# Optimization experiments

Hardware: AMD Instinct MI355X
Metric: run time of the kernel (lower is better)

The kernel has to match this reference:

```python
import jax, jax.numpy as jnp
import numpy as np

BETA, HIDDEN, C_DIM = 512, 512, 256
HP, WP, B = 64, 64, 64


def setup_inputs() -> dict:
    key = jax.random.key(0)
    ks = jax.random.split(key, 8)
    s = 0.02
    return {
        "V": jax.random.normal(ks[0], (HP, WP, C_DIM, B), dtype=jnp.float32),
        "h_t": jax.random.normal(ks[1], (B, 1, HIDDEN), dtype=jnp.float32),
        "W_h_w": jax.random.normal(ks[2], (BETA, HIDDEN), dtype=jnp.float32) * s,
        "W_h_b": jax.random.normal(ks[3], (BETA,), dtype=jnp.float32) * s,
        "W_w": jax.random.normal(ks[4], (BETA, C_DIM), dtype=jnp.float32) * s,
        "W_b": jax.random.normal(ks[5], (BETA,), dtype=jnp.float32) * s,
        "beta_w": jax.random.normal(ks[6], (1, BETA), dtype=jnp.float32) * s,
        "beta_b": jax.random.normal(ks[7], (1,), dtype=jnp.float32) * s,
    }


def reference(V, h_t, W_h_w, W_h_b, W_w, W_b, beta_w, beta_b):
    Hp, Wp, C, batch = V.shape
    # [B, HW, C]
    V_new = jnp.transpose(V, (3, 0, 1, 2)).reshape(batch, Hp * Wp, C)
    # U_T = W_h(h_t) + W(V_new): [B,1,beta] + [B,HW,beta]
    U_T = (h_t @ W_h_w.T + W_h_b) + (V_new @ W_w.T + W_b)
    # E_t: [B, HW, 1]
    E_t = jnp.tanh(U_T) @ beta_w.T + beta_b
    # softmax over the HW positions (dim=1), then transpose -> [B, 1, HW]
    A_t = jax.nn.softmax(E_t, axis=1)
    # weighted sum: [B, 1, C]
    C_T = jnp.einsum('bsk,bsc->bkc', A_t, V_new)
    return C_T
```

## Files before the change

### kernel.cpp

```cpp
#include <hip/hip_runtime.h>

typedef float f32x4 __attribute__((ext_vector_type(4)));
typedef short s16x8 __attribute__((ext_vector_type(8)));
typedef unsigned int u32;
typedef u32 u32x4 __attribute__((ext_vector_type(4)));
typedef unsigned long long u64;
typedef unsigned short ush;

#define CD    256
#define NB    64
#define NBETA 512
#define NHID  512
#define PPB   32

__device__ __forceinline__ ush f2bf(float x) {
    u32 u = __builtin_bit_cast(u32, x);
    u += 0x7fffu + ((u >> 16) & 1u);
    return (ush)(u >> 16);
}
__device__ __forceinline__ float bf2f(ush h) {
    u32 u = ((u32)h) << 16;
    return __builtin_bit_cast(float, u);
}
__device__ __forceinline__ u32 cvtpk(float lo, float hi) {
    u32 r;
    asm("v_cvt_pk_bf16_f32 %0, %1, %2" : "=v"(r) : "v"(lo), "v"(hi));
    return r;
}
__device__ __forceinline__ float fexp2(float x) {
    float r;
    asm("v_exp_f32 %0, %1" : "=v"(r) : "v"(x));
    return r;
}

__global__ __launch_bounds__(512) void prep_kernel(
    const float* __restrict__ h_t, const float* __restrict__ W_h_w,
    const float* __restrict__ W_h_b, const float* __restrict__ W_w,
    const float* __restrict__ W_b,
    ush* __restrict__ hws, ush* __restrict__ wwb)
{
    const int blk = blockIdx.x;
    const int tid = threadIdx.x;
    if (blk < NB) {
        __shared__ float hrow[NHID];
        hrow[tid] = h_t[blk * NHID + tid];
        __syncthreads();
        const float* wr = W_h_w + tid * NHID;
        float a0 = 0.f, a1 = 0.f, a2 = 0.f, a3 = 0.f;
        #pragma unroll 4
        for (int h = 0; h < NHID; h += 4) {
            f32x4 wv = *(const f32x4*)(wr + h);
            a0 = fmaf(wv.x, hrow[h], a0);
            a1 = fmaf(wv.y, hrow[h + 1], a1);
            a2 = fmaf(wv.z, hrow[h + 2], a2);
            a3 = fmaf(wv.w, hrow[h + 3], a3);
        }
        float acc = (a0 + a1) + (a2 + a3) + W_h_b[tid] + W_b[tid];
        hws[blk * NBETA + tid] = f2bf(acc);
    } else {
        const int idx = ((blk - NB) * 512 + tid) * 8;
        f32x4 a = *(const f32x4*)(W_w + idx);
        f32x4 b = *(const f32x4*)(W_w + idx + 4);
        s16x8 pk;
        pk[0] = (short)f2bf(a.x); pk[1] = (short)f2bf(a.y);
        pk[2] = (short)f2bf(a.z); pk[3] = (short)f2bf(a.w);
        pk[4] = (short)f2bf(b.x); pk[5] = (short)f2bf(b.y);
        pk[6] = (short)f2bf(b.z); pk[7] = (short)f2bf(b.w);
        *(s16x8*)(wwb + idx) = pk;
    }
}

__global__ __launch_bounds__(512, 2) void fused(
    const float* __restrict__ V,
    const ush* __restrict__ wwb,
    const ush* __restrict__ hws,
    const float* __restrict__ beta_w,
    const float* __restrict__ beta_b,
    float* __restrict__ num,
    float* __restrict__ lsum)
{
    __shared__ __align__(16) char VtB[3][16384];
    __shared__ float nbS[NBETA];
    __shared__ __align__(16) float ew2[2][32][12];

    const int tid = threadIdx.x;
    const int l = tid & 63, w = tid >> 6, g = l >> 4, r = l & 15;
    const int bl = tid & 31, cs = tid >> 5;
    const int bh = blockIdx.x & 1, chunk = blockIdx.x >> 1;

    nbS[tid] = -2.f * beta_w[tid];
    const float bbias = beta_b[0];

    float base = 0.f;
    #pragma unroll
    for (int m = 0; m < 4; ++m) {
        f32x4 t = *(const f32x4*)(beta_w + w * 64 + m * 16 + g * 4);
        base += (t.x + t.y) + (t.z + t.w);
    }

    const ush* wbase = wwb + (size_t)(w * 64 + r) * CD + g * 8;
    s16x8 a[4][8];
    #pragma unroll
    for (int m = 0; m < 4; ++m)
        #pragma unroll
        for (int ks = 0; ks < 8; ++ks)
            a[m][ks] = *(const s16x8*)(wbase + m * (16 * CD) + ks * 32);

    const ush* hbase = hws + (size_t)(bh * 32 + r) * NBETA + w * 64 + g * 4;
    u64 ua[4][2];
    #pragma unroll
    for (int m = 0; m < 4; ++m)
        #pragma unroll
        for (int n = 0; n < 2; ++n)
            ua[m][n] = *(const u64*)(hbase + n * (16 * NBETA) + m * 16);

    const int p0 = chunk * PPB;
    const float* vbase = V + (size_t)p0 * (CD * NB) + bh * 32 + bl;
    const int wswz = (bl & 15) << 4;
    const int rswz = r << 4;

    float cacc[16];
    #pragma unroll
    for (int j = 0; j < 16; ++j) cacc[j] = 0.f;
    float lacc = 0.f;

    float nv[16];
    {
        #pragma unroll
        for (int j = 0; j < 16; ++j)
            nv[j] = __builtin_nontemporal_load(vbase + (cs * 16 + j) * NB);
        char* db = VtB[0] + bl * 512;
        u32x4 pk0 = {cvtpk(nv[0], nv[1]), cvtpk(nv[2], nv[3]),
                     cvtpk(nv[4], nv[5]), cvtpk(nv[6], nv[7])};
        *(u32x4*)(db + ((cs * 32) ^ wswz)) = pk0;
        u32x4 pk1 = {cvtpk(nv[8], nv[9]), cvtpk(nv[10], nv[11]),
                     cvtpk(nv[12], nv[13]), cvtpk(nv[14], nv[15])};
        *(u32x4*)(db + ((cs * 32 + 16) ^ wswz)) = pk1;
    }
    {
        const float* vp = vbase + (size_t)(CD * NB);
        #pragma unroll
        for (int j = 0; j < 16; ++j)
            nv[j] = __builtin_nontemporal_load(vp + (cs * 16 + j) * NB);
    }
    __syncthreads();

    int cur = 0, nxt = 16384;
    for (int i = 0; i < PPB; ++i) {
        const char* vt = VtB[0] + cur;

        if (i + 1 < PPB) {
            char* db = VtB[0] + nxt + bl * 512;
            u32x4 pk0 = {cvtpk(nv[0], nv[1]), cvtpk(nv[2], nv[3]),
                         cvtpk(nv[4], nv[5]), cvtpk(nv[6], nv[7])};
            *(u32x4*)(db + ((cs * 32) ^ wswz)) = pk0;
            u32x4 pk1 = {cvtpk(nv[8], nv[9]), cvtpk(nv[10], nv[11]),
                         cvtpk(nv[12], nv[13]), cvtpk(nv[14], nv[15])};
            *(u32x4*)(db + ((cs * 32 + 16) ^ wswz)) = pk1;
        }
        if (i + 2 < PPB) {
            const float* vp = vbase + (size_t)(i + 2) * (CD * NB);
            #pragma unroll
            for (int j = 0; j < 16; ++j)
                nv[j] = __builtin_nontemporal_load(vp + (cs * 16 + j) * NB);
        }

        const char* vrow = vt + r * 512;

        f32x4 acc0[4];
        #pragma unroll
        for (int m = 0; m < 4; ++m) {
            u64 h = ua[m][0];
            acc0[m] = (f32x4){bf2f((ush)h), bf2f((ush)(h >> 16)),
                              bf2f((ush)(h >> 32)), bf2f((ush)(h >> 48))};
        }
        #pragma unroll
        for (int ks = 0; ks < 8; ++ks) {
            const int off = ((ks << 6) | (g << 4)) ^ rswz;
            s16x8 b0 = *(const s16x8*)(vrow + off);
            #pragma unroll
            for (int m = 0; m < 4; ++m)
                acc0[m] = __builtin_amdgcn_mfma_f32_16x16x32_bf16(a[m][ks], b0, acc0[m], 0, 0, 0);
        }
        float pe0 = base;
        #pragma unroll
        for (int m = 0; m < 4; ++m) {
            f32x4 nbv = *(const f32x4*)(&nbS[w * 64 + m * 16 + g * 4]);
            #pragma unroll
            for (int q = 0; q < 4; ++q) {
                float s = __builtin_amdgcn_rcpf(
                    1.f + fexp2(acc0[m][q] * 2.8853900817779268f));
                pe0 = fmaf(nbv[q], s, pe0);
            }
        }

        f32x4 acc1[4];
        #pragma unroll
        for (int m = 0; m < 4; ++m) {
            u64 h = ua[m][1];
            acc1[m] = (f32x4){bf2f((ush)h), bf2f((ush)(h >> 16)),
                              bf2f((ush)(h >> 32)), bf2f((ush)(h >> 48))};
        }
        #pragma unroll
        for (int ks = 0; ks < 8; ++ks) {
            const int off = ((ks << 6) | (g << 4)) ^ rswz;
            s16x8 b1 = *(const s16x8*)(vrow + 8192 + off);
            #pragma unroll
            for (int m = 0; m < 4; ++m)
                acc1[m] = __builtin_amdgcn_mfma_f32_16x16x32_bf16(a[m][ks], b1, acc1[m], 0, 0, 0);
        }
        float pe1 = base;
        #pragma unroll
        for (int m = 0; m < 4; ++m) {
            f32x4 nbv = *(const f32x4*)(&nbS[w * 64 + m * 16 + g * 4]);
            #pragma unroll
            for (int q = 0; q < 4; ++q) {
                float s = __builtin_amdgcn_rcpf(
                    1.f + fexp2(acc1[m][q] * 2.8853900817779268f));
                pe1 = fmaf(nbv[q], s, pe1);
            }
        }

        pe0 += __shfl_xor(pe0, 16, 64); pe0 += __shfl_xor(pe0, 32, 64);
        pe1 += __shfl_xor(pe1, 16, 64); pe1 += __shfl_xor(pe1, 32, 64);
        if (l < 16) { ew2[i & 1][l][w] = pe0; ew2[i & 1][16 + l][w] = pe1; }

        __syncthreads();

        const float* er = &ew2[i & 1][bl][0];
        f32x4 s4 = *(const f32x4*)er + *(const f32x4*)(er + 4);
        float e = bbias + (s4.x + s4.y) + (s4.z + s4.w);
        float wgt = __expf(e);
        lacc += wgt;
        const char* vb = vt + bl * 512;
        #pragma unroll
        for (int k = 0; k < 2; ++k) {
            s16x8 v = *(const s16x8*)(vb + ((cs * 32 + k * 16) ^ wswz));
            #pragma unroll
            for (int j = 0; j < 8; ++j)
                cacc[k * 8 + j] = fmaf(wgt, bf2f((ush)v[j]), cacc[k * 8 + j]);
        }

        cur = nxt;
        nxt += 16384;
        if (nxt == 49152) nxt = 0;
    }

    float* np = num + (size_t)blockIdx.x * (32 * CD) + bl * CD + cs * 16;
    #pragma unroll
    for (int k = 0; k < 4; ++k)
        *(f32x4*)(np + k * 4) =
            (f32x4){cacc[k * 4], cacc[k * 4 + 1], cacc[k * 4 + 2], cacc[k * 4 + 3]};
    if (cs == 0) lsum[blockIdx.x * 32 + bl] = lacc;
}

__global__ __launch_bounds__(256) void combine4(
    const float* __restrict__ num, const float* __restrict__ lsum,
    float* __restrict__ out)
{
    __shared__ float rs[4][64];
    __shared__ float rl[4][64];
    const int b = blockIdx.x >> 2, cq = blockIdx.x & 3;
    const int bh = b >> 5, blr = b & 31;
    const int cl = threadIdx.x & 63, kq = threadIdx.x >> 6;

    float s = 0.f, ls = 0.f;
    #pragma unroll 4
    for (int ch = kq * 32; ch < kq * 32 + 32; ++ch) {
        const int blk = ch * 2 + bh;
        s += num[(size_t)blk * (32 * CD) + blr * CD + cq * 64 + cl];
        ls += lsum[blk * 32 + blr];
    }
    rs[kq][cl] = s; rl[kq][cl] = ls;
    __syncthreads();
    if (kq == 0) {
        float sn = rs[0][cl] + rs[1][cl] + rs[2][cl] + rs[3][cl];
        float sl = rl[0][cl] + rl[1][cl] + rl[2][cl] + rl[3][cl];
        out[b * CD + cq * 64 + cl] = sn / sl;
    }
}

extern "C" void kernel_launch(void* const* d_in, const int* in_sizes, int n_in,
                              void* d_out, int out_size, void* d_ws, size_t ws_size,
                              hipStream_t stream)
{
    (void)in_sizes; (void)n_in; (void)out_size; (void)ws_size;
    const float* V      = (const float*)d_in[0];
    const float* h_t    = (const float*)d_in[1];
    const float* W_h_w  = (const float*)d_in[2];
    const float* W_h_b  = (const float*)d_in[3];
    const float* W_w    = (const float*)d_in[4];
    const float* W_b    = (const float*)d_in[5];
    const float* beta_w = (const float*)d_in[6];
    const float* beta_b = (const float*)d_in[7];

    char* ws = (char*)d_ws;
    ush*   wwb = (ush*)ws;
    ush*   hws = (ush*)(ws + 262144);
    float* num = (float*)(ws + 262144 + 65536);
    float* lsm = (float*)(ws + 262144 + 65536 + 8388608);

    hipLaunchKernelGGL(prep_kernel, dim3(96), dim3(512), 0, stream,
                       h_t, W_h_w, W_h_b, W_w, W_b, hws, wwb);
    hipLaunchKernelGGL(fused, dim3(256), dim3(512), 0, stream,
                       V, wwb, hws, beta_w, beta_b, num, lsm);
    hipLaunchKernelGGL(combine4, dim3(256), dim3(256), 0, stream,
                       num, lsm, (float*)d_out);
}
```

Before: 151.6 us.

## Keep packed V in registers for weighted sum and software-pipeline the loop

Each position's V tile is now packed to bf16 once and kept in registers. The weighted accumulation for that position is deferred into the next iteration and reads those registers instead of LDS. This lets the LDS ring shrink from three buffers to two with an unrolled ping-pong, and drops the per-iteration LDS reads of V in the accumulation phase. The next position's global loads are also split around the first MFMA chain, and s_setprio is raised during the MFMA sections. In exchange, register pressure rises from the extra packed vectors, and the unrolled macro body makes the code larger.

```diff
diff --git a/kernel.cpp b/kernel.cpp
--- a/kernel.cpp
+++ b/kernel.cpp
@@ -21,6 +21,12 @@
 __device__ __forceinline__ float bf2f(ush h) {
     u32 u = ((u32)h) << 16;
     return __builtin_bit_cast(float, u);
+}
+__device__ __forceinline__ float bflo(u32 u) {
+    return __builtin_bit_cast(float, u << 16);
+}
+__device__ __forceinline__ float bfhi(u32 u) {
+    return __builtin_bit_cast(float, u & 0xFFFF0000u);
 }
 __device__ __forceinline__ u32 cvtpk(float lo, float hi) {
     u32 r;
@@ -79,7 +85,7 @@
     float* __restrict__ num,
     float* __restrict__ lsum)
 {
-    __shared__ __align__(16) char VtB[3][16384];
+    __shared__ __align__(16) char VtB[2][16384];
     __shared__ float nbS[NBETA];
     __shared__ __align__(16) float ew2[2][32][12];
 
@@ -125,19 +131,19 @@
     float lacc = 0.f;
 
     float nv[16];
+    u32x4 pkA[2], pkB[2];
+
     {
         #pragma unroll
         for (int j = 0; j < 16; ++j)
             nv[j] = __builtin_nontemporal_load(vbase + (cs * 16 + j) * NB);
+        pkB[0] = (u32x4){cvtpk(nv[0], nv[1]), cvtpk(nv[2], nv[3]),
+                         cvtpk(nv[4], nv[5]), cvtpk(nv[6], nv[7])};
+        pkB[1] = (u32x4){cvtpk(nv[8], nv[9]), cvtpk(nv[10], nv[11]),
+                         cvtpk(nv[12], nv[13]), cvtpk(nv[14], nv[15])};
         char* db = VtB[0] + bl * 512;
-        u32x4 pk0 = {cvtpk(nv[0], nv[1]), cvtpk(nv[2], nv[3]),
-                     cvtpk(nv[4], nv[5]), cvtpk(nv[6], nv[7])};
-        *(u32x4*)(db + ((cs * 32) ^ wswz)) = pk0;
-        u32x4 pk1 = {cvtpk(nv[8], nv[9]), cvtpk(nv[10], nv[11]),
-                     cvtpk(nv[12], nv[13]), cvtpk(nv[14], nv[15])};
-        *(u32x4*)(db + ((cs * 32 + 16) ^ wswz)) = pk1;
-    }
-    {
+        *(u32x4*)(db + ((cs * 32) ^ wswz)) = pkB[0];
+        *(u32x4*)(db + ((cs * 32 + 16) ^ wswz)) = pkB[1];
         const float* vp = vbase + (size_t)(CD * NB);
         #pragma unroll
         for (int j = 0; j < 16; ++j)
@@ -145,106 +151,123 @@
     }
     __syncthreads();
 
-    int cur = 0, nxt = 16384;
-    for (int i = 0; i < PPB; ++i) {
-        const char* vt = VtB[0] + cur;
-
-        if (i + 1 < PPB) {
-            char* db = VtB[0] + nxt + bl * 512;
-            u32x4 pk0 = {cvtpk(nv[0], nv[1]), cvtpk(nv[2], nv[3]),
-                         cvtpk(nv[4], nv[5]), cvtpk(nv[6], nv[7])};
-            *(u32x4*)(db + ((cs * 32) ^ wswz)) = pk0;
-            u32x4 pk1 = {cvtpk(nv[8], nv[9]), cvtpk(nv[10], nv[11]),
-                         cvtpk(nv[12], nv[13]), cvtpk(nv[14], nv[15])};
-            *(u32x4*)(db + ((cs * 32 + 16) ^ wswz)) = pk1;
-        }
-        if (i + 2 < PPB) {
-            const float* vp = vbase + (size_t)(i + 2) * (CD * NB);
-            #pragma unroll
-            for (int j = 0; j < 16; ++j)
-                nv[j] = __builtin_nontemporal_load(vp + (cs * 16 + j) * NB);
-        }
-
-        const char* vrow = vt + r * 512;
-
-        f32x4 acc0[4];
-        #pragma unroll
-        for (int m = 0; m < 4; ++m) {
-            u64 h = ua[m][0];
-            acc0[m] = (f32x4){bf2f((ush)h), bf2f((ush)(h >> 16)),
-                              bf2f((ush)(h >> 32)), bf2f((ush)(h >> 48))};
-        }
-        #pragma unroll
-        for (int ks = 0; ks < 8; ++ks) {
-            const int off = ((ks << 6) | (g << 4)) ^ rswz;
-            s16x8 b0 = *(const s16x8*)(vrow + off);
-            #pragma unroll
-            for (int m = 0; m < 4; ++m)
-                acc0[m] = __builtin_amdgcn_mfma_f32_16x16x32_bf16(a[m][ks], b0, acc0[m], 0, 0, 0);
-        }
-        float pe0 = base;
-        #pragma unroll
-        for (int m = 0; m < 4; ++m) {
-            f32x4 nbv = *(const f32x4*)(&nbS[w * 64 + m * 16 + g * 4]);
-            #pragma unroll
-            for (int q = 0; q < 4; ++q) {
-                float s = __builtin_amdgcn_rcpf(
-                    1.f + fexp2(acc0[m][q] * 2.8853900817779268f));
-                pe0 = fmaf(nbv[q], s, pe0);
-            }
-        }
-
-        f32x4 acc1[4];
-        #pragma unroll
-        for (int m = 0; m < 4; ++m) {
-            u64 h = ua[m][1];
-            acc1[m] = (f32x4){bf2f((ush)h), bf2f((ush)(h >> 16)),
-                              bf2f((ush)(h >> 32)), bf2f((ush)(h >> 48))};
-        }
-        #pragma unroll
-        for (int ks = 0; ks < 8; ++ks) {
-            const int off = ((ks << 6) | (g << 4)) ^ rswz;
-            s16x8 b1 = *(const s16x8*)(vrow + 8192 + off);
-            #pragma unroll
-            for (int m = 0; m < 4; ++m)
-                acc1[m] = __builtin_amdgcn_mfma_f32_16x16x32_bf16(a[m][ks], b1, acc1[m], 0, 0, 0);
-        }
-        float pe1 = base;
-        #pragma unroll
-        for (int m = 0; m < 4; ++m) {
-            f32x4 nbv = *(const f32x4*)(&nbS[w * 64 + m * 16 + g * 4]);
-            #pragma unroll
-            for (int q = 0; q < 4; ++q) {
-                float s = __builtin_amdgcn_rcpf(
-                    1.f + fexp2(acc1[m][q] * 2.8853900817779268f));
-                pe1 = fmaf(nbv[q], s, pe1);
-            }
-        }
-
-        pe0 += __shfl_xor(pe0, 16, 64); pe0 += __shfl_xor(pe0, 32, 64);
-        pe1 += __shfl_xor(pe1, 16, 64); pe1 += __shfl_xor(pe1, 32, 64);
-        if (l < 16) { ew2[i & 1][l][w] = pe0; ew2[i & 1][16 + l][w] = pe1; }
-
-        __syncthreads();
-
-        const float* er = &ew2[i & 1][bl][0];
-        f32x4 s4 = *(const f32x4*)er + *(const f32x4*)(er + 4);
-        float e = bbias + (s4.x + s4.y) + (s4.z + s4.w);
-        float wgt = __expf(e);
-        lacc += wgt;
-        const char* vb = vt + bl * 512;
-        #pragma unroll
-        for (int k = 0; k < 2; ++k) {
-            s16x8 v = *(const s16x8*)(vb + ((cs * 32 + k * 16) ^ wswz));
-            #pragma unroll
-            for (int j = 0; j < 8; ++j)
-                cacc[k * 8 + j] = fmaf(wgt, bf2f((ush)v[j]), cacc[k * 8 + j]);
-        }
-
-        cur = nxt;
-        nxt += 16384;
-        if (nxt == 49152) nxt = 0;
-    }
+#define WSUM(PK, EP)                                                          \
+    {                                                                         \
+        const float* er = &ew2[EP][bl][0];                                    \
+        f32x4 sa = *(const f32x4*)er;                                         \
+        f32x4 sb = *(const f32x4*)(er + 4);                                   \
+        float e = bbias + ((sa.x + sa.y) + (sa.z + sa.w))                     \
+                        + ((sb.x + sb.y) + (sb.z + sb.w));                    \
+        float wgt = __expf(e);                                                \
+        lacc += wgt;                                                          \
+        _Pragma("unroll")                                                     \
+        for (int k = 0; k < 2; ++k)                                           \
+            _Pragma("unroll")                                                 \
+            for (int w2 = 0; w2 < 4; ++w2) {                                  \
+                u32 u = PK[k][w2];                                            \
+                cacc[k * 8 + w2 * 2]     = fmaf(wgt, bflo(u), cacc[k * 8 + w2 * 2]);     \
+                cacc[k * 8 + w2 * 2 + 1] = fmaf(wgt, bfhi(u), cacc[k * 8 + w2 * 2 + 1]); \
+            }                                                                 \
+    }
+
+#define BODY(I, PK, BC, BN, EC, EP)                                           \
+    {                                                                         \
+        const int i_ = (I);                                                   \
+        if (i_ > 0) WSUM(PK, EP)                                              \
+        if (i_ + 1 < PPB) {                                                   \
+            PK[0] = (u32x4){cvtpk(nv[0], nv[1]), cvtpk(nv[2], nv[3]),         \
+                            cvtpk(nv[4], nv[5]), cvtpk(nv[6], nv[7])};        \
+            PK[1] = (u32x4){cvtpk(nv[8], nv[9]), cvtpk(nv[10], nv[11]),       \
+                            cvtpk(nv[12], nv[13]), cvtpk(nv[14], nv[15])};    \
+            char* db = VtB[BN] + bl * 512;                                    \
+            *(u32x4*)(db + ((cs * 32) ^ wswz)) = PK[0];                       \
+            *(u32x4*)(db + ((cs * 32 + 16) ^ wswz)) = PK[1];                  \
+        }                                                                     \
+        if (i_ + 2 < PPB) {                                                   \
+            const float* vp = vbase + (size_t)(i_ + 2) * (CD * NB);           \
+            _Pragma("unroll")                                                 \
+            for (int j = 0; j < 8; ++j)                                       \
+                nv[j] = __builtin_nontemporal_load(vp + (cs * 16 + j) * NB);  \
+        }                                                                     \
+        const char* vrow = VtB[BC] + r * 512;                                 \
+        f32x4 acc0[4];                                                        \
+        _Pragma("unroll")                                                     \
+        for (int m = 0; m < 4; ++m) {                                         \
+            u64 h = ua[m][0];                                                 \
+            acc0[m] = (f32x4){bf2f((ush)h), bf2f((ush)(h >> 16)),             \
+                              bf2f((ush)(h >> 32)), bf2f((ush)(h >> 48))};    \
+        }                                                                     \
+        __builtin_amdgcn_s_setprio(1);                                        \
+        _Pragma("unroll")                                                     \
+        for (int ks = 0; ks < 8; ++ks) {                                      \
+            const int off = ((ks << 6) | (g << 4)) ^ rswz;                    \
+            s16x8 b0 = *(const s16x8*)(vrow + off);                           \
+            _Pragma("unroll")                                                 \
+            for (int m = 0; m < 4; ++m)                                       \
+                acc0[m] = __builtin_amdgcn_mfma_f32_16x16x32_bf16(            \
+                    a[m][ks], b0, acc0[m], 0, 0, 0);                          \
+        }                                                                     \
+        __builtin_amdgcn_s_setprio(0);                                        \
+        if (i_ + 2 < PPB) {                                                   \
+            const float* vp = vbase + (size_t)(i_ + 2) * (CD * NB);           \
+            _Pragma("unroll")                                                 \
+            for (int j = 8; j < 16; ++j)                                      \
+                nv[j] = __builtin_nontemporal_load(vp + (cs * 16 + j) * NB);  \
+        }                                                                     \
+        float pe0 = base;                                                     \
+        _Pragma("unroll")                                                     \
+        for (int m = 0; m < 4; ++m) {                                         \
+            f32x4 nbv = *(const f32x4*)(&nbS[w * 64 + m * 16 + g * 4]);       \
+            _Pragma("unroll")                                                 \
+            for (int q = 0; q < 4; ++q) {                                     \
+                float s = __builtin_amdgcn_rcpf(                              \
+                    1.f + fexp2(acc0[m][q] * 2.8853900817779268f));           \
+                pe0 = fmaf(nbv[q], s, pe0);                                   \
+            }                                                                 \
+        }                                                                     \
+        f32x4 acc1[4];                                                        \
+        _Pragma("unroll")                                                     \
+        for (int m = 0; m < 4; ++m) {                                         \
+            u64 h = ua[m][1];                                                 \
+            acc1[m] = (f32x4){bf2f((ush)h), bf2f((ush)(h >> 16)),             \
+                              bf2f((ush)(h >> 32)), bf2f((ush)(h >> 48))};    \
+        }                                                                     \
+        __builtin_amdgcn_s_setprio(1);                                        \
+        _Pragma("unroll")                                                     \
+        for (int ks = 0; ks < 8; ++ks) {                                      \
+            const int off = ((ks << 6) | (g << 4)) ^ rswz;                    \
+            s16x8 b1 = *(const s16x8*)(vrow + 8192 + off);                    \
+            _Pragma("unroll")                                                 \
+            for (int m = 0; m < 4; ++m)                                       \
+                acc1[m] = __builtin_amdgcn_mfma_f32_16x16x32_bf16(            \
+                    a[m][ks], b1, acc1[m], 0, 0, 0);                          \
+        }                                                                     \
+        __builtin_amdgcn_s_setprio(0);                                        \
+        float pe1 = base;                                                     \
+        _Pragma("unroll")                                                     \
+        for (int m = 0; m < 4; ++m) {                                         \
+            f32x4 nbv = *(const f32x4*)(&nbS[w * 64 + m * 16 + g * 4]);       \
+            _Pragma("unroll")                                                 \
+            for (int q = 0; q < 4; ++q) {                                     \
+                float s = __builtin_amdgcn_rcpf(                              \
+                    1.f + fexp2(acc1[m][q] * 2.8853900817779268f));           \
+                pe1 = fmaf(nbv[q], s, pe1);                                   \
+            }                                                                 \
+        }                                                                     \
+        pe0 += __shfl_xor(pe0, 16, 64); pe0 += __shfl_xor(pe0, 32, 64);       \
+        pe1 += __shfl_xor(pe1, 16, 64); pe1 += __shfl_xor(pe1, 32, 64);       \
+        if (l < 16) { ew2[EC][l][w] = pe0; ew2[EC][16 + l][w] = pe1; }        \
+        __syncthreads();                                                      \
+    }
+
+    for (int ii = 0; ii < PPB; ii += 2) {
+        BODY(ii,     pkA, 0, 1, 0, 1)
+        BODY(ii + 1, pkB, 1, 0, 1, 0)
+    }
+    WSUM(pkA, 1)
+
+#undef BODY
+#undef WSUM
 
     float* np = num + (size_t)blockIdx.x * (32 * CD) + bl * CD + cs * 16;
     #pragma unroll
```

After: 177.0 us. 1.17x slower.
